# Kernel optimization log

Hardware: AMD Instinct MI355X
Metric: run time of the kernel (lower is better)

The kernel has to match this reference:

```python
import jax, jax.numpy as jnp
import numpy as np

D_MODEL = 256
INPUT_DIM = 63
NUM_CLASSES = 13
NUM_LAYERS = 4
D_STATE = 128
D_CONV = 4
D_INNER = 512          # expand * d_model
HEADDIM = 64
NHEADS = D_INNER // HEADDIM  # 8
NGROUPS = 1
CONV_DIM = D_INNER + 2 * NGROUPS * D_STATE   # 768
D_IN_PROJ = 2 * D_INNER + 2 * NGROUPS * D_STATE + NHEADS  # 1160
BATCH, SEQLEN = 8, 2048


def setup_inputs() -> dict:
    key = jax.random.key(0)
    ks = jax.random.split(key, 12)
    s = 0.02
    f32 = jnp.float32
    # dt_bias init as in mamba2: inverse-softplus of dt in [1e-3, 1e-1]
    dt = jnp.exp(jax.random.uniform(ks[6], (NUM_LAYERS, NHEADS), f32) * (np.log(0.1) - np.log(0.001)) + np.log(0.001))
    dt_bias = dt + jnp.log(-jnp.expm1(-dt))
    A_log = jnp.log(jax.random.uniform(ks[7], (NUM_LAYERS, NHEADS), f32, 1.0, 16.0))
    return {
        "x": jax.random.normal(ks[0], (BATCH, SEQLEN, INPUT_DIM), f32),
        "in_w": jax.random.normal(ks[1], (D_MODEL, INPUT_DIM), f32) * s,
        "in_b": jnp.zeros((D_MODEL,), f32),
        "ln_in_g": jnp.ones((D_MODEL,), f32),
        "ln_in_b": jnp.zeros((D_MODEL,), f32),
        "inproj_w": jax.random.normal(ks[2], (NUM_LAYERS, D_IN_PROJ, D_MODEL), f32) * s,
        "conv_w": jax.random.normal(ks[3], (NUM_LAYERS, CONV_DIM, D_CONV), f32) * 0.2,
        "conv_b": jnp.zeros((NUM_LAYERS, CONV_DIM), f32),
        "dt_bias": dt_bias,
        "A_log": A_log,
        "D": jnp.ones((NUM_LAYERS, NHEADS), f32),
        "norm_w": jnp.ones((NUM_LAYERS, D_INNER), f32),
        "outproj_w": jax.random.normal(ks[4], (NUM_LAYERS, D_MODEL, D_INNER), f32) * s,
        "ln_g": jnp.ones((NUM_LAYERS, D_MODEL), f32),
        "ln_b": jnp.zeros((NUM_LAYERS, D_MODEL), f32),
        "out_w": jax.random.normal(ks[5], (NUM_CLASSES, D_MODEL), f32) * s,
        "out_b": jnp.zeros((NUM_CLASSES,), f32),
    }


def layernorm(x, g, b, eps=1e-5):
    m = jnp.mean(x, -1, keepdims=True)
    v = jnp.mean(jnp.square(x - m), -1, keepdims=True)
    return (x - m) * jax.lax.rsqrt(v + eps) * g + b


def mamba2_block(x, w_in, cw, cb, dtb, Alog, Dp, nw, w_out):
    # x: (b, l, d_model)
    b, l, _ = x.shape
    zxbcdt = jnp.einsum('bld,ed->ble', x, w_in)                 # (b,l,1160)
    z = zxbcdt[..., :D_INNER]                                   # (b,l,512)
    xBC = zxbcdt[..., D_INNER:D_INNER + CONV_DIM]               # (b,l,768)
    dt = jax.nn.softplus(zxbcdt[..., D_INNER + CONV_DIM:] + dtb)  # (b,l,8)
    # causal depthwise conv1d + silu
    xp = jnp.pad(xBC, ((0, 0), (D_CONV - 1, 0), (0, 0)))
    kern = cw.T[:, None, :]                                     # (K,1,C)
    xBC = jax.lax.conv_general_dilated(
        xp, kern, (1,), 'VALID',
        dimension_numbers=('NWC', 'WIO', 'NWC'),
        feature_group_count=CONV_DIM)
    xBC = jax.nn.silu(xBC + cb)
    xin = xBC[..., :D_INNER].reshape(b, l, NHEADS, HEADDIM)     # (b,l,h,p)
    Bm = xBC[..., D_INNER:D_INNER + D_STATE]                    # (b,l,n)
    Cm = xBC[..., D_INNER + D_STATE:]                           # (b,l,n)
    A = -jnp.exp(Alog)                                          # (h,)
    dA = jnp.exp(dt * A)                                        # (b,l,h)
    dtx = dt[..., None] * xin                                   # (b,l,h,p)

    def step(state, inp):
        dA_t, dtx_t, B_t, C_t = inp                             # (b,h),(b,h,p),(b,n),(b,n)
        state = state * dA_t[..., None, None] + dtx_t[..., None] * B_t[:, None, None, :]
        y_t = jnp.einsum('bhpn,bn->bhp', state, C_t)
        return state, y_t

    state0 = jnp.zeros((b, NHEADS, HEADDIM, D_STATE), x.dtype)
    _, ys = jax.lax.scan(step, state0, (
        dA.transpose(1, 0, 2), dtx.transpose(1, 0, 2, 3),
        Bm.transpose(1, 0, 2), Cm.transpose(1, 0, 2)))
    y = ys.transpose(1, 0, 2, 3) + Dp[:, None] * xin            # (b,l,h,p)
    y = y.reshape(b, l, D_INNER)
    # gated RMSNorm (norm_before_gate=False): rmsnorm(y * silu(z)) * w
    y = y * jax.nn.silu(z)
    y = y * jax.lax.rsqrt(jnp.mean(jnp.square(y), -1, keepdims=True) + 1e-5) * nw
    return jnp.einsum('ble,de->bld', y, w_out)


def reference(x, in_w, in_b, ln_in_g, ln_in_b, inproj_w, conv_w, conv_b,
              dt_bias, A_log, D, norm_w, outproj_w, ln_g, ln_b, out_w, out_b):
    # input projection (dropout is identity in eval mode)
    h = layernorm(jnp.einsum('bli,di->bld', x, in_w) + in_b, ln_in_g, ln_in_b)
    for i in range(NUM_LAYERS):
        res = h
        h = mamba2_block(h, inproj_w[i], conv_w[i], conv_b[i], dt_bias[i],
                         A_log[i], D[i], norm_w[i], outproj_w[i])
        h = layernorm(h + res, ln_g[i], ln_b[i])
    logits = jnp.einsum('bld,cd->blc', h, out_w) + out_b
    return logits.transpose(1, 0, 2)  # (T, N, C) for CTC
```

## Files before the change

kernel.cpp:

```cpp
#include <hip/hip_runtime.h>
#include <math.h>


#define NTOK   16384
#define DMODEL 256
#define DINNER 512
#define DSTATE 128
#define NHEADS 8
#define HEADDIM 64
#define CONVDIM 768
#define DINPROJ 1288
#define NPADIN 1408
#define Q      128
#define NCHUNK 16
#define NBC    128

typedef __attribute__((ext_vector_type(8))) short bf16x8v;
typedef __attribute__((ext_vector_type(4))) float f32x4;
typedef __attribute__((ext_vector_type(8))) unsigned short ush8;
typedef __attribute__((ext_vector_type(4))) unsigned short ush4;

__device__ __forceinline__ float siluf_(float x){ return x / (1.f + expf(-x)); }

__device__ __forceinline__ unsigned short f2bf(float x){
  union { float f; unsigned u; } v; v.f = x;
  unsigned r = v.u + 0x7FFF + ((v.u >> 16) & 1);
  return (unsigned short)(r >> 16);
}
__device__ __forceinline__ float bf2f(unsigned short u){
  union { unsigned u; float f; } v; v.u = ((unsigned)u) << 16; return v.f;
}
__device__ __forceinline__ void g2lds16(const void* g, void* l){
  __builtin_amdgcn_global_load_lds(
      (const __attribute__((address_space(1))) unsigned int*)g,
      (__attribute__((address_space(3))) unsigned int*)l, 16, 0, 0);
}

__global__ __launch_bounds__(256) void k_cast_x(const float* __restrict__ x,
    unsigned short* __restrict__ xb){
  int idx = blockIdx.x*256 + threadIdx.x;
  int col = idx & 63, row = idx >> 6;
  xb[idx] = (col < 63) ? f2bf(x[(size_t)row*63 + col]) : 0;
}
__global__ __launch_bounds__(256) void k_cast_inw(const float* __restrict__ w,
    unsigned short* __restrict__ wb){
  int idx = blockIdx.x*256 + threadIdx.x;
  int k = idx & 63, n = idx >> 6;
  wb[idx] = (k < 63) ? f2bf(w[(size_t)n*63 + k]) : 0;
}
__global__ __launch_bounds__(256) void k_cast_pad(const float* __restrict__ w,
    unsigned short* __restrict__ wb, int Nsrc, int Npad, int K, int total){
  int idx = blockIdx.x*256 + threadIdx.x;
  if (idx >= total) return;
  int k = idx % K;
  int n = (idx / K) % Npad;
  int l = idx / (K*Npad);
  float v = (n < Nsrc) ? w[((size_t)l*Nsrc + n)*K + k] : 0.f;
  wb[idx] = f2bf(v);
}

__global__ __launch_bounds__(256) void gemm_ln(const unsigned short* __restrict__ A,
    const unsigned short* __restrict__ W, float* __restrict__ h,
    unsigned short* __restrict__ hb, const float* __restrict__ g,
    const float* __restrict__ be, int K, int addres){
  __shared__ unsigned short As[64*64];
  __shared__ unsigned short Ws[256*64];
  __shared__ float redS[4][64], redS2[4][64];
  int m0 = blockIdx.x * 64;
  int t = threadIdx.x;
  int wave = t >> 6, lane = t & 63;
  int lr = lane & 15, lk = lane >> 4;
  f32x4 acc[4][4] = {};
  for (int k0=0; k0<K; k0+=64){
    #pragma unroll
    for (int i=0;i<2;i++){
      int seg = i*256 + t;
      int row = seg >> 3, c8 = (seg&7)*8;
      g2lds16(A + (size_t)(m0+row)*K + k0 + c8, (char*)As + seg*16);
    }
    #pragma unroll
    for (int i=0;i<8;i++){
      int seg = i*256 + t;
      int row = seg >> 3, c8 = (seg&7)*8;
      g2lds16(W + (size_t)row*K + k0 + c8, (char*)Ws + seg*16);
    }
    __syncthreads();
    #pragma unroll
    for (int kk=0;kk<2;kk++){
      bf16x8v wf[4], af[4];
      #pragma unroll
      for (int ci=0;ci<4;ci++)
// ... 22 lines not shown
      }
      #pragma unroll
      for (int j=0;j<4;j++){ float v = acc[ci][ti][j]; pS[ti]+=v; pS2[ti]+=v*v; }
    }
  }
  #pragma unroll
  for (int ti=0;ti<4;ti++){
    pS[ti]  += __shfl_xor(pS[ti],16);  pS[ti]  += __shfl_xor(pS[ti],32);
    pS2[ti] += __shfl_xor(pS2[ti],16); pS2[ti] += __shfl_xor(pS2[ti],32);
  }
  if (lk == 0){
    #pragma unroll
    for (int ti=0;ti<4;ti++){ redS[wave][ti*16+lr] = pS[ti]; redS2[wave][ti*16+lr] = pS2[ti]; }
  }
  __syncthreads();
  #pragma unroll
  for (int ti=0;ti<4;ti++){
    int rloc = ti*16 + lr;
    float S  = redS[0][rloc]+redS[1][rloc]+redS[2][rloc]+redS[3][rloc];
    float S2 = redS2[0][rloc]+redS2[1][rloc]+redS2[2][rloc]+redS2[3][rloc];
    float mean = S*(1.f/256.f);
    float var  = S2*(1.f/256.f) - mean*mean;
    float r = rsqrtf(var + 1e-5f);
    int token = m0 + rloc;
    #pragma unroll
    for (int ci=0;ci<4;ci++){
      int col = wave*64 + ci*16 + lk*4;
      float o[4];
      #pragma unroll
      for (int j=0;j<4;j++) o[j] = (acc[ci][ti][j]-mean)*r*g[col+j] + be[col+j];
      *(float4*)&h[(size_t)token*256 + col] = make_float4(o[0],o[1],o[2],o[3]);
      ush4 ub = {f2bf(o[0]),f2bf(o[1]),f2bf(o[2]),f2bf(o[3])};
      *(ush4*)&hb[(size_t)token*256 + col] = ub;
    }
  }
}

__global__ __launch_bounds__(256) void gemm_in(const unsigned short* __restrict__ A,
    const unsigned short* __restrict__ W, unsigned short* __restrict__ zxb,
    const float* __restrict__ dt_bias, const float* __restrict__ A_log,
    float* __restrict__ dtg, float* __restrict__ Lag, float* __restrict__ Tg,
    float* __restrict__ wgb){
  __shared__ unsigned short As[128*64];
  __shared__ unsigned short Ws[128*64];
  int m0 = blockIdx.x * 128;
  int n0 = blockIdx.y * 128;
  int t = threadIdx.x;
  int wave = t >> 6, lane = t & 63;
  int wt = wave >> 1, wn = wave & 1;
  int lr = lane & 15, lk = lane >> 4;
  f32x4 acc[4][4] = {};
  for (int k0=0; k0<DMODEL; k0+=64){
    #pragma unroll
    for (int i=0;i<4;i++){
      int seg = i*256 + t;
      int row = seg >> 3, c8 = (seg&7)*8;
      g2lds16(A + (size_t)(m0+row)*DMODEL + k0 + c8, (char*)As + seg*16);
      g2lds16(W + (size_t)(n0+row)*DMODEL + k0 + c8, (char*)Ws + seg*16);
    }
    __syncthreads();
    #pragma unroll
    for (int kk=0;kk<2;kk++){
      bf16x8v wf[4], af[4];
      #pragma unroll
      for (int ci=0;ci<4;ci++)
        wf[ci] = *(const bf16x8v*)&Ws[(wn*64 + ci*16 + lr)*64 + kk*32 + lk*8];
      #pragma unroll
      for (int ti=0;ti<4;ti++)
        af[ti] = *(const bf16x8v*)&As[(wt*64 + ti*16 + lr)*64 + kk*32 + lk*8];
      #pragma unroll
      for (int ci=0;ci<4;ci++)
        #pragma unroll
        for (int ti=0;ti<4;ti++)
          acc[ci][ti] = __builtin_amdgcn_mfma_f32_16x16x32_bf16(wf[ci], af[ti], acc[ci][ti],0,0,0);
    }
    __syncthreads();
  }
  #pragma unroll
  for (int ci=0;ci<4;ci++){
    int col4 = n0 + wn*64 + ci*16 + lk*4;
    if (col4 < DINPROJ){
      #pragma unroll
      for (int ti=0;ti<4;ti++){
        int token = m0 + wt*64 + ti*16 + lr;
        ush4 ub = {f2bf(acc[ci][ti][0]),f2bf(acc[ci][ti][1]),
                   f2bf(acc[ci][ti][2]),f2bf(acc[ci][ti][3])};
        *(ush4*)&zxb[(size_t)token*DINPROJ + col4] = ub;
      }
    }
  }
  if (blockIdx.y == 10){
    float* dls = (float*)As;
    if (wn == 0 && lk < 2){
      #pragma unroll
      for (int ti=0;ti<4;ti++){
        int token = wt*64 + ti*16 + lr;
        #pragma unroll
        for (int j=0;j<4;j++) dls[token*8 + lk*4 + j] = acc[0][ti][j];
      }
    }
    __syncthreads();
    int bc = blockIdx.x;
    int rowc = m0;
    #pragma unroll
    for (int hi=0; hi<2; hi++){
      int hh = wave*2 + hi;
      float Aa = -expf(A_log[hh]);
      float bias = dt_bias[hh];
      int t0 = 2*lane, t1 = 2*lane+1;
      float r0v = dls[t0*8+hh] + bias;
      float r1v = dls[t1*8+hh] + bias;
      float d0 = (r0v > 20.f) ? r0v : log1pf(expf(r0v));
      float d1 = (r1v > 20.f) ? r1v : log1pf(expf(r1v));
      float v0 = d0*Aa, v1 = d1*Aa;
      float run = v0 + v1;
      #pragma unroll
      for (int off=1; off<64; off<<=1){
        float nb = __shfl_up(run, off);
        if (lane >= off) run += nb;
      }
      float La1 = run;
      float La0 = run - v1;
      float La_last = __shfl(run, 63);
      dtg[(size_t)(rowc+t0)*8 + hh] = d0;
      dtg[(size_t)(rowc+t1)*8 + hh] = d1;
      Lag[(size_t)(rowc+t0)*8 + hh] = La0;
      Lag[(size_t)(rowc+t1)*8 + hh] = La1;
      wgb[(size_t)(bc*8+hh)*Q + t0] = expf(La_last - La0) * d0;
      wgb[(size_t)(bc*8+hh)*Q + t1] = expf(La_last - La1) * d1;
      if (lane == 63) Tg[bc*8 + hh] = expf(La1);
    }
  }
}

__global__ __launch_bounds__(256) void k_conv(const unsigned short* __restrict__ zxb,
    const float* __restrict__ cw, const float* __restrict__ cb,
    unsigned short* __restrict__ xbcb, unsigned short* __restrict__ Xt,
    unsigned short* __restrict__ Bt){
  int tid = threadIdx.x;
  int c0 = (blockIdx.x * 8 + (tid & 7)) * 8;
  int tg = blockIdx.y * 32 + (tid >> 3);
  int r0 = tg * 8;
  int l0 = r0 & 2047;
  float kw[4][8], bias[8];
  #pragma unroll
  for (int j=0;j<8;j++){
    float4 k4 = *(const float4*)&cw[(c0+j)*4];
    kw[0][j]=k4.x; kw[1][j]=k4.y; kw[2][j]=k4.z; kw[3][j]=k4.w;
    bias[j] = cb[c0+j];
  }
  float zv[11][8];
  #pragma unroll
  for (int i=0;i<11;i++){
    if (l0 - 3 + i >= 0){
      ush8 v = *(const ush8*)&zxb[(size_t)(r0-3+i)*DINPROJ + 512 + c0];
      #pragma unroll
      for (int j=0;j<8;j++) zv[i][j] = bf2f(v[j]);
    } else {
      #pragma unroll
      for (int j=0;j<8;j++) zv[i][j] = 0.f;
    }
  }
  unsigned short ob[8][8];
  #pragma unroll
  for (int tt=0;tt<8;tt++){
    #pragma unroll
    for (int j=0;j<8;j++){
      float acc = bias[j] + zv[tt][j]*kw[0][j] + zv[tt+1][j]*kw[1][j]
                + zv[tt+2][j]*kw[2][j] + zv[tt+3][j]*kw[3][j];
      ob[tt][j] = f2bf(siluf_(acc));
    }
    *(ush8*)&xbcb[(size_t)(r0+tt)*CONVDIM + c0] = *(ush8*)ob[tt];
  }
  if (c0 < 640){
    int bc = r0 >> 7, s0 = r0 & 127;
    #pragma unroll
    for (int j=0;j<8;j++){
      ush8 col = {ob[0][j],ob[1][j],ob[2][j],ob[3][j],ob[4][j],ob[5][j],ob[6][j],ob[7][j]};
      int d = c0 + j;
      unsigned short* dst = (d < 512)
          ? (Xt + ((size_t)bc*512 + d)*Q + s0)
          : (Bt + ((size_t)bc*128 + (d-512))*Q + s0);
      *(ush8*)dst = col;
    }
  }
}

__global__ __launch_bounds__(256) void k_cbp1(const unsigned short* __restrict__ xbcb,
    const unsigned short* __restrict__ Bt, const unsigned short* __restrict__ Xt,
    const float* __restrict__ wg, unsigned short* __restrict__ CBb,
    float* __restrict__ states){
  __shared__ char smem[52736];
  int tid = threadIdx.x;
  int bc = blockIdx.x;
  int wave = tid >> 6, lane = tid & 63;
  int lr = lane & 15, lk = lane >> 4;
  if (blockIdx.y == 8){
    unsigned short* Cs = (unsigned short*)smem;
    unsigned short* Bs = (unsigned short*)(smem + 16384);
    int rowc = bc * Q;
    int wS = wave >> 1, wT = wave & 1;
    f32x4 acc[4][4] = {};
    for (int k0 = 0; k0 < DSTATE; k0 += 64){
      #pragma unroll
      for (int i=0;i<4;i++){
        int seg = i*256 + tid;
        int row = seg >> 3;
        int c8  = (seg & 7) * 8;
        g2lds16(xbcb + (size_t)(rowc+row)*CONVDIM + 640 + k0 + c8, Cs + seg*8);
        g2lds16(xbcb + (size_t)(rowc+row)*CONVDIM + 512 + k0 + c8, Bs + seg*8);
      }
      __syncthreads();
      #pragma unroll
      for (int kk=0; kk<2; kk++){
        bf16x8v bS[4], cT[4];
        #pragma unroll
        for (int si=0;si<4;si++)
          bS[si] = *(const bf16x8v*)&Bs[(wS*64 + si*16 + lr)*64 + kk*32 + lk*8];
        #pragma unroll
        for (int ti=0;ti<4;ti++)
          cT[ti] = *(const bf16x8v*)&Cs[(wT*64 + ti*16 + lr)*64 + kk*32 + lk*8];
        #pragma unroll
        for (int si=0;si<4;si++)
          #pragma unroll
// ... 28 lines not shown
      int n = seg >> 4;
      int s8 = (seg & 15) * 8;
      ush8 u = *(const ush8*)&Bt[(size_t)bc*128*Q + n*Q + s8];
      ush8 o;
      #pragma unroll
      for (int j=0;j<8;j++) o[j] = f2bf(bf2f(u[j]) * wv[s8+j]);
      *(ush8*)&Bw[n*136 + s8] = o;
    }
    #pragma unroll
    for (int it=0; it<4; it++){
      int seg = it*256 + tid;
      int p = seg >> 4;
      int s8 = (seg & 15) * 8;
      *(ush8*)&Xs[p*136 + s8] = *(const ush8*)&Xt[(size_t)bc*512*Q + (h*64+p)*Q + s8];
    }
    __syncthreads();
    int wn = wave >> 1, wp = wave & 1;
    f32x4 acc[4][2] = {};
    #pragma unroll
    for (int ks=0; ks<4; ks++){
      bf16x8v a[4], x[2];
      #pragma unroll
      for (int mi=0;mi<4;mi++)
        a[mi] = *(const bf16x8v*)&Bw[(wn*64 + mi*16 + lr)*136 + ks*32 + lk*8];
      #pragma unroll
      for (int ni=0;ni<2;ni++)
        x[ni] = *(const bf16x8v*)&Xs[(wp*32 + ni*16 + lr)*136 + ks*32 + lk*8];
      #pragma unroll
      for (int mi=0;mi<4;mi++)
        #pragma unroll
        for (int ni=0;ni<2;ni++)
          acc[mi][ni] = __builtin_amdgcn_mfma_f32_16x16x32_bf16(a[mi], x[ni], acc[mi][ni], 0, 0, 0);
    }
    float* st = states + ((size_t)(b*8+h)*16 + c) * (DSTATE*HEADDIM);
    #pragma unroll
    for (int mi=0;mi<4;mi++)
      #pragma unroll
      for (int ni=0;ni<2;ni++){
        int p = wp*32 + ni*16 + lr;
        int nb = wn*64 + mi*16 + lk*4;
        *(f32x4*)&st[p*DSTATE + nb] = acc[mi][ni];
      }
  }
}

__global__ __launch_bounds__(256) void k_pass2(const float* __restrict__ states,
    const float* __restrict__ T, unsigned short* __restrict__ st0b){
  int e = blockIdx.x*256 + threadIdx.x;
  int bh = e >> 13;
  int np = e & 8191;
  int b = bh >> 3, h = bh & 7;
  size_t base = (size_t)bh * NCHUNK * 8192 + np;
  float run = 0.f;
  #pragma unroll
  for (int c=0; c<NCHUNK; c++){
    float g = states[base + (size_t)c*8192];
    st0b[base + (size_t)c*8192] = f2bf(run);
    run = fmaf(T[(b*NCHUNK+c)*8 + h], run, g);
  }
}

__global__ __launch_bounds__(256) void k_pass3(const unsigned short* __restrict__ xbcb,
    const unsigned short* __restrict__ Xt, const unsigned short* __restrict__ CBb,
    const unsigned short* __restrict__ st0b, const float* __restrict__ dt,
    const float* __restrict__ La, unsigned short* __restrict__ yssmb){
  int bc = blockIdx.x, h = blockIdx.y;
  int b = bc >> 4, c = bc & 15;
  int rowc = bc * Q;
  int tid = threadIdx.x;
  __shared__ unsigned short bufA[128*136];
  __shared__ unsigned short bufB[64*136];
  __shared__ float La_s[Q], dt_s[Q], eLa_s[Q];
  if (tid < Q){
    float Lv = La[(size_t)(rowc+tid)*8 + h];
    La_s[tid] = Lv;
    dt_s[tid] = dt[(size_t)(rowc+tid)*8 + h];
    eLa_s[tid] = expf(Lv);
  }
  #pragma unroll
  for (int it=0; it<8; it++){
    int seg = it*256 + tid;
    int tt = seg >> 4;
    int n8 = (seg & 15) * 8;
    *(ush8*)&bufA[tt*136 + n8] = *(const ush8*)&xbcb[(size_t)(rowc+tt)*CONVDIM + 640 + n8];
  }
  const unsigned short* S0 = st0b + ((size_t)(b*8+h)*16 + c) * 8192;
  #pragma unroll
  for (int it=0; it<4; it++){
    int seg = it*256 + tid;
// ... 50 lines not shown
  for (int it=0; it<4; it++){
    int seg = it*256 + tid;
    int p = seg >> 4;
    int s8 = (seg & 15) * 8;
    *(ush8*)&bufB[p*136 + s8] = *(const ush8*)&Xt[(size_t)bc*512*Q + (h*64+p)*Q + s8];
  }
  __syncthreads();
  #pragma unroll
  for (int ks=0; ks<4; ks++){
    bf16x8v xf[2], mf[4];
    #pragma unroll
    for (int pi=0;pi<2;pi++)
      xf[pi] = *(const bf16x8v*)&bufB[(wp*32 + pi*16 + lr)*136 + ks*32 + lk*8];
    #pragma unroll
    for (int ti=0;ti<4;ti++)
      mf[ti] = *(const bf16x8v*)&bufA[(wt*64 + ti*16 + lr)*136 + ks*32 + lk*8];
    #pragma unroll
    for (int pi=0;pi<2;pi++)
      #pragma unroll
      for (int ti=0;ti<4;ti++)
        acc[pi][ti] = __builtin_amdgcn_mfma_f32_16x16x32_bf16(xf[pi], mf[ti], acc[pi][ti],0,0,0);
  }
  #pragma unroll
  for (int pi=0;pi<2;pi++){
    int p4 = wp*32 + pi*16 + lk*4;
    #pragma unroll
    for (int ti=0;ti<4;ti++){
      int tt = wt*64 + ti*16 + lr;
      ush4 ub = {f2bf(acc[pi][ti][0]),f2bf(acc[pi][ti][1]),
                 f2bf(acc[pi][ti][2]),f2bf(acc[pi][ti][3])};
      *(ush4*)&yssmb[(size_t)(rowc+tt)*DINNER + h*64 + p4] = ub;
    }
  }
}

__global__ __launch_bounds__(64) void k_gate_norm(const unsigned short* __restrict__ yssmb,
    const unsigned short* __restrict__ xbcb, const unsigned short* __restrict__ zxb,
    const float* __restrict__ Dp, const float* __restrict__ nw,
    unsigned short* __restrict__ outb){
  int row = blockIdx.x;
  int t = threadIdx.x;
  int d0 = t*8;
  ush8 ys = *(const ush8*)&yssmb[(size_t)row*DINNER + d0];
  ush8 xi = *(const ush8*)&xbcb[(size_t)row*CONVDIM + d0];
  ush8 z8 = *(const ush8*)&zxb[(size_t)row*DINPROJ + d0];
  float Dh = Dp[d0 >> 6];
  float v[8];
  float s2 = 0.f;
  #pragma unroll
  for (int j=0;j<8;j++){
    v[j] = fmaf(Dh, bf2f(xi[j]), bf2f(ys[j])) * siluf_(bf2f(z8[j]));
    s2 += v[j]*v[j];
  }
  #pragma unroll
  for (int off=1; off<64; off<<=1) s2 += __shfl_xor(s2, off);
  float r = rsqrtf(s2*(1.f/512.f) + 1e-5f);
  unsigned short ub[8];
  #pragma unroll
  for (int j=0;j<8;j++) ub[j] = f2bf(v[j]*r*nw[d0+j]);
  *(ush8*)&outb[(size_t)row*DINNER + d0] = *(ush8*)ub;
}

__global__ __launch_bounds__(256) void k_logits(const unsigned short* __restrict__ hb,
    const float* __restrict__ ow, const float* __restrict__ ob,
    float* __restrict__ out){
  int idx = blockIdx.x*256 + threadIdx.x;
  if (idx >= 2048*8*13) return;
  int c = idx % 13;
  int bb = (idx/13) & 7;
  int l = idx / 104;
  const ush8* hr = (const ush8*)(hb + (size_t)(bb*2048 + l)*256);
  const float4* wr = (const float4*)(ow + c*256);
  float acc = ob[c];
  #pragma unroll 4
  for (int d=0; d<32; d++){
    ush8 a = hr[d];
    float4 w0 = wr[d*2], w1 = wr[d*2+1];
    acc += bf2f(a[0])*w0.x + bf2f(a[1])*w0.y + bf2f(a[2])*w0.z + bf2f(a[3])*w0.w
         + bf2f(a[4])*w1.x + bf2f(a[5])*w1.y + bf2f(a[6])*w1.z + bf2f(a[7])*w1.w;
  }
  out[idx] = acc;
}

extern "C" void kernel_launch(void* const* d_in, const int* in_sizes, int n_in,
                              void* d_out, int out_size, void* d_ws, size_t ws_size,
                              hipStream_t stream) {
  const float* x        = (const float*)d_in[0];
  const float* in_w     = (const float*)d_in[1];
  const float* ln_in_g  = (const float*)d_in[3];
  const float* ln_in_b  = (const float*)d_in[4];
  const float* inproj_w = (const float*)d_in[5];
  const float* conv_w   = (const float*)d_in[6];
  const float* conv_b   = (const float*)d_in[7];
  const float* dt_bias  = (const float*)d_in[8];
  const float* A_log    = (const float*)d_in[9];
  const float* Dp       = (const float*)d_in[10];
  const float* norm_w   = (const float*)d_in[11];
  const float* outproj_w= (const float*)d_in[12];
  const float* ln_g     = (const float*)d_in[13];
  const float* ln_b     = (const float*)d_in[14];
  const float* out_w    = (const float*)d_in[15];
  const float* out_b    = (const float*)d_in[16];

  float* ws = (float*)d_ws;
  float* h      = ws;
  float* dtg    = ws + 4325376;
  float* Lag    = ws + 4456448;
  float* Tg     = ws + 4587520;
  float* wg     = ws + 4588544;
  float* statesF= ws + 5637120;
  unsigned short* zxb   = (unsigned short*)(ws + 14025728);
  unsigned short* xbcb  = (unsigned short*)(ws + 24577024);
  unsigned short* Xt    = (unsigned short*)(ws + 30868480);
  unsigned short* Bt    = (unsigned short*)(ws + 35062784);
  unsigned short* CBb   = (unsigned short*)(ws + 36111360);
  unsigned short* st0b  = (unsigned short*)(ws + 37159936);
  unsigned short* yssmb = (unsigned short*)(ws + 41354240);
  unsigned short* ynormb= (unsigned short*)(ws + 45548544);
  unsigned short* hb    = (unsigned short*)(ws + 49742848);
  unsigned short* xb    = (unsigned short*)(ws + 51840000);
  unsigned short* wxb   = (unsigned short*)(ws + 52364288);
  unsigned short* wbin  = (unsigned short*)(ws + 52372480);
  unsigned short* wbout = (unsigned short*)(ws + 53093376);

  k_cast_x<<<NTOK*64/256, 256, 0, stream>>>(x, xb);
  k_cast_inw<<<DMODEL*64/256, 256, 0, stream>>>(in_w, wxb);
  k_cast_pad<<<(4*NPADIN*DMODEL + 255)/256, 256, 0, stream>>>(
      inproj_w, wbin, DINPROJ, NPADIN, DMODEL, 4*NPADIN*DMODEL);
  k_cast_pad<<<(4*DMODEL*DINNER + 255)/256, 256, 0, stream>>>(
      outproj_w, wbout, DMODEL, DMODEL, DINNER, 4*DMODEL*DINNER);
  gemm_ln<<<NTOK/64, 256, 0, stream>>>(xb, wxb, h, hb, ln_in_g, ln_in_b, 64, 0);

  for (int i=0; i<4; i++){
    gemm_in<<<dim3(NTOK/128, NPADIN/128), 256, 0, stream>>>(
        hb, wbin + (size_t)i*NPADIN*DMODEL, zxb,
        dt_bias + i*NHEADS, A_log + i*NHEADS, dtg, Lag, Tg, wg);
    k_conv<<<dim3(12, 64), 256, 0, stream>>>(zxb, conv_w + (size_t)i*CONVDIM*4,
        conv_b + i*CONVDIM, xbcb, Xt, Bt);
    k_cbp1<<<dim3(NBC, 9), 256, 0, stream>>>(xbcb, Bt, Xt, wg, CBb, statesF);
    k_pass2<<<2048, 256, 0, stream>>>(statesF, Tg, st0b);
    k_pass3<<<dim3(NBC, NHEADS), 256, 0, stream>>>(xbcb, Xt, CBb, st0b, dtg, Lag, yssmb);
    k_gate_norm<<<NTOK, 64, 0, stream>>>(yssmb, xbcb, zxb, Dp + i*NHEADS,
        norm_w + i*DINNER, ynormb);
    gemm_ln<<<NTOK/64, 256, 0, stream>>>(ynormb, wbout + (size_t)i*DMODEL*DINNER,
        h, hb, ln_g + i*DMODEL, ln_b + i*DMODEL, 512, 1);
  }

  k_logits<<<(2048*8*13 + 255)/256, 256, 0, stream>>>(hb, out_w, out_b, (float*)d_out);
}
```

Before: 617.3 us.

## Fuse depthwise conv into in-projection GEMM epilogue and merge cast kernels

The causal depthwise conv plus SiLU is computed inside the in-projection GEMM epilogue for the xBC column tiles, reading the tile from shared memory. The three preceding rows come from a small recomputed dot product against the previous tokens' hidden state, so the full zxbcdt intermediate no longer needs to be written to and re-read from global memory. Only z is stored, in a compact buffer. This removes the separate k_conv launch and its traffic, and the four weight/input cast kernels are merged into one launch. The cost is extra shared memory, a scalar halo recompute, and a heavier epilogue in the GEMM.

```diff
diff --git a/kernel.cpp b/kernel.cpp
--- a/kernel.cpp
+++ b/kernel.cpp
@@ -36,27 +36,33 @@
       (__attribute__((address_space(3))) unsigned int*)l, 16, 0, 0);
 }
 
-__global__ __launch_bounds__(256) void k_cast_x(const float* __restrict__ x,
-    unsigned short* __restrict__ xb){
+__global__ __launch_bounds__(256) void k_cast_all(const float* __restrict__ x,
+    const float* __restrict__ in_w, const float* __restrict__ inproj_w,
+    const float* __restrict__ outproj_w, unsigned short* __restrict__ xb,
+    unsigned short* __restrict__ wxb, unsigned short* __restrict__ wbin,
+    unsigned short* __restrict__ wbout){
   int idx = blockIdx.x*256 + threadIdx.x;
-  int col = idx & 63, row = idx >> 6;
-  xb[idx] = (col < 63) ? f2bf(x[(size_t)row*63 + col]) : 0;
-}
-__global__ __launch_bounds__(256) void k_cast_inw(const float* __restrict__ w,
-    unsigned short* __restrict__ wb){
-  int idx = blockIdx.x*256 + threadIdx.x;
-  int k = idx & 63, n = idx >> 6;
-  wb[idx] = (k < 63) ? f2bf(w[(size_t)n*63 + k]) : 0;
-}
-__global__ __launch_bounds__(256) void k_cast_pad(const float* __restrict__ w,
-    unsigned short* __restrict__ wb, int Nsrc, int Npad, int K, int total){
-  int idx = blockIdx.x*256 + threadIdx.x;
-  if (idx >= total) return;
-  int k = idx % K;
-  int n = (idx / K) % Npad;
-  int l = idx / (K*Npad);
-  float v = (n < Nsrc) ? w[((size_t)l*Nsrc + n)*K + k] : 0.f;
-  wb[idx] = f2bf(v);
+  if (idx < 1048576){
+    int col = idx & 63, row = idx >> 6;
+    xb[idx] = (col < 63) ? f2bf(x[(size_t)row*63 + col]) : 0;
+    return;
+  }
+  idx -= 1048576;
+  if (idx < 16384){
+    int k = idx & 63, n = idx >> 6;
+    wxb[idx] = (k < 63) ? f2bf(in_w[(size_t)n*63 + k]) : 0;
+    return;
+  }
+  idx -= 16384;
+  if (idx < 1441792){
+    int k = idx & 255;
+    int n = (idx >> 8) % NPADIN;
+    int l = idx / (256*NPADIN);
+    wbin[idx] = (n < DINPROJ) ? f2bf(inproj_w[((size_t)l*DINPROJ + n)*256 + k]) : 0;
+    return;
+  }
+  idx -= 1441792;
+  if (idx < 524288) wbout[idx] = f2bf(outproj_w[idx]);
 }
 
 __global__ __launch_bounds__(256) void gemm_ln(const unsigned short* __restrict__ A,
@@ -150,12 +156,16 @@
 }
 
 __global__ __launch_bounds__(256) void gemm_in(const unsigned short* __restrict__ A,
-    const unsigned short* __restrict__ W, unsigned short* __restrict__ zxb,
+    const unsigned short* __restrict__ W, unsigned short* __restrict__ zb,
+    unsigned short* __restrict__ xbcb, unsigned short* __restrict__ Xt,
+    unsigned short* __restrict__ Bt,
+    const float* __restrict__ cw, const float* __restrict__ cb,
     const float* __restrict__ dt_bias, const float* __restrict__ A_log,
     float* __restrict__ dtg, float* __restrict__ Lag, float* __restrict__ Tg,
     float* __restrict__ wgb){
-  __shared__ unsigned short As[128*64];
-  __shared__ unsigned short Ws[128*64];
+  __shared__ char smem[37376];
+  unsigned short* As = (unsigned short*)smem;
+  unsigned short* Ws = (unsigned short*)(smem + 16384);
   int m0 = blockIdx.x * 128;
   int n0 = blockIdx.y * 128;
   int t = threadIdx.x;
@@ -189,21 +199,99 @@
     }
     __syncthreads();
   }
-  #pragma unroll
-  for (int ci=0;ci<4;ci++){
-    int col4 = n0 + wn*64 + ci*16 + lk*4;
-    if (col4 < DINPROJ){
+  int ytile = blockIdx.y;
+  if (ytile < 4){
+    #pragma unroll
+    for (int ci=0;ci<4;ci++){
+      int col4 = n0 + wn*64 + ci*16 + lk*4;
       #pragma unroll
       for (int ti=0;ti<4;ti++){
         int token = m0 + wt*64 + ti*16 + lr;
         ush4 ub = {f2bf(acc[ci][ti][0]),f2bf(acc[ci][ti][1]),
                    f2bf(acc[ci][ti][2]),f2bf(acc[ci][ti][3])};
-        *(ush4*)&zxb[(size_t)token*DINPROJ + col4] = ub;
-      }
-    }
-  }
-  if (blockIdx.y == 10){
-    float* dls = (float*)As;
+        *(ush4*)&zb[(size_t)token*512 + col4] = ub;
+      }
+    }
+  } else if (ytile < 10){
+    unsigned short* zraw = (unsigned short*)smem;
+    unsigned short* hb3  = (unsigned short*)(smem + 35632);
+    bool haveprev = (m0 & 2047) != 0;
+    if (t < 96){
+      int r = t >> 5, c8 = (t & 31) * 8;
+      ush8 v = {0,0,0,0,0,0,0,0};
+      if (haveprev) v = *(const ush8*)&A[(size_t)(m0-3+r)*DMODEL + c8];
+      *(ush8*)&hb3[r*256 + c8] = v;
+    }
+    #pragma unroll
+    for (int ci=0;ci<4;ci++){
+      int cl = wn*64 + ci*16 + lk*4;
+      #pragma unroll
+      for (int ti=0;ti<4;ti++){
+        int tl = wt*64 + ti*16 + lr;
+        ush4 ub = {f2bf(acc[ci][ti][0]),f2bf(acc[ci][ti][1]),
+                   f2bf(acc[ci][ti][2]),f2bf(acc[ci][ti][3])};
+        *(ush4*)&zraw[(tl+3)*136 + cl] = ub;
+      }
+    }
+    __syncthreads();
+    for (int idx = t; idx < 384; idx += 256){
+      int r = idx >> 7, c = idx & 127;
+      float dot = 0.f;
+      if (haveprev){
+        const ush8* wr8 = (const ush8*)&W[(size_t)(n0+c)*DMODEL];
+        const ush8* hr8 = (const ush8*)&hb3[r*256];
+        #pragma unroll 8
+        for (int k8=0;k8<32;k8++){
+          ush8 wv = wr8[k8], hv = hr8[k8];
+          #pragma unroll
+          for (int j=0;j<8;j++) dot += bf2f(hv[j]) * bf2f(wv[j]);
+        }
+      }
+      zraw[r*136 + c] = f2bf(dot);
+    }
+    __syncthreads();
+    int cl0 = (t & 15)*8;
+    int tl0 = (t >> 4)*8;
+    int ch0 = (n0 - 512) + cl0;
+    float kw[4][8], bias[8];
+    #pragma unroll
+    for (int j=0;j<8;j++){
+      float4 k4 = *(const float4*)&cw[(ch0+j)*4];
+      kw[0][j]=k4.x; kw[1][j]=k4.y; kw[2][j]=k4.z; kw[3][j]=k4.w;
+      bias[j] = cb[ch0+j];
+    }
+    float zv[11][8];
+    #pragma unroll
+    for (int i=0;i<11;i++){
+      ush8 v = *(const ush8*)&zraw[(tl0+i)*136 + cl0];
+      #pragma unroll
+      for (int j=0;j<8;j++) zv[i][j] = bf2f(v[j]);
+    }
+    unsigned short ob[8][8];
+    #pragma unroll
+    for (int tt=0;tt<8;tt++){
+      #pragma unroll
+      for (int j=0;j<8;j++){
+        float a = bias[j] + zv[tt][j]*kw[0][j] + zv[tt+1][j]*kw[1][j]
+                + zv[tt+2][j]*kw[2][j] + zv[tt+3][j]*kw[3][j];
+        ob[tt][j] = f2bf(siluf_(a));
+      }
+      *(ush8*)&xbcb[(size_t)(m0+tl0+tt)*CONVDIM + ch0] = *(ush8*)ob[tt];
+    }
+    if (ch0 < 640){
+      int bc = m0 >> 7;
+      #pragma unroll
+      for (int j=0;j<8;j++){
+        int d = ch0 + j;
+        ush8 col = {ob[0][j],ob[1][j],ob[2][j],ob[3][j],ob[4][j],ob[5][j],ob[6][j],ob[7][j]};
+        unsigned short* dst = (d < 512)
+            ? (Xt + ((size_t)bc*512 + d)*Q + tl0)
+            : (Bt + ((size_t)bc*128 + (d-512))*Q + tl0);
+        *(ush8*)dst = col;
+      }
+    }
+  } else {
+    float* dls = (float*)smem;
     if (wn == 0 && lk < 2){
       #pragma unroll
       for (int ti=0;ti<4;ti++){
@@ -242,59 +330,6 @@
       wgb[(size_t)(bc*8+hh)*Q + t0] = expf(La_last - La0) * d0;
       wgb[(size_t)(bc*8+hh)*Q + t1] = expf(La_last - La1) * d1;
       if (lane == 63) Tg[bc*8 + hh] = expf(La1);
-    }
-  }
-}
-
-__global__ __launch_bounds__(256) void k_conv(const unsigned short* __restrict__ zxb,
-    const float* __restrict__ cw, const float* __restrict__ cb,
-    unsigned short* __restrict__ xbcb, unsigned short* __restrict__ Xt,
-    unsigned short* __restrict__ Bt){
-  int tid = threadIdx.x;
-  int c0 = (blockIdx.x * 8 + (tid & 7)) * 8;
-  int tg = blockIdx.y * 32 + (tid >> 3);
-  int r0 = tg * 8;
-  int l0 = r0 & 2047;
-  float kw[4][8], bias[8];
-  #pragma unroll
-  for (int j=0;j<8;j++){
-    float4 k4 = *(const float4*)&cw[(c0+j)*4];
-    kw[0][j]=k4.x; kw[1][j]=k4.y; kw[2][j]=k4.z; kw[3][j]=k4.w;
-    bias[j] = cb[c0+j];
-  }
-  float zv[11][8];
-  #pragma unroll
-  for (int i=0;i<11;i++){
-    if (l0 - 3 + i >= 0){
-      ush8 v = *(const ush8*)&zxb[(size_t)(r0-3+i)*DINPROJ + 512 + c0];
-      #pragma unroll
-      for (int j=0;j<8;j++) zv[i][j] = bf2f(v[j]);
-    } else {
-      #pragma unroll
-      for (int j=0;j<8;j++) zv[i][j] = 0.f;
-    }
-  }
-  unsigned short ob[8][8];
-  #pragma unroll
-  for (int tt=0;tt<8;tt++){
-    #pragma unroll
-    for (int j=0;j<8;j++){
-      float acc = bias[j] + zv[tt][j]*kw[0][j] + zv[tt+1][j]*kw[1][j]
-                + zv[tt+2][j]*kw[2][j] + zv[tt+3][j]*kw[3][j];
-      ob[tt][j] = f2bf(siluf_(acc));
-    }
-    *(ush8*)&xbcb[(size_t)(r0+tt)*CONVDIM + c0] = *(ush8*)ob[tt];
-  }
-  if (c0 < 640){
-    int bc = r0 >> 7, s0 = r0 & 127;
-    #pragma unroll
-    for (int j=0;j<8;j++){
-      ush8 col = {ob[0][j],ob[1][j],ob[2][j],ob[3][j],ob[4][j],ob[5][j],ob[6][j],ob[7][j]};
-      int d = c0 + j;
-      unsigned short* dst = (d < 512)
-          ? (Xt + ((size_t)bc*512 + d)*Q + s0)
-          : (Bt + ((size_t)bc*128 + (d-512))*Q + s0);
-      *(ush8*)dst = col;
     }
   }
 }
@@ -539,7 +574,7 @@
 }
 
 __global__ __launch_bounds__(64) void k_gate_norm(const unsigned short* __restrict__ yssmb,
-    const unsigned short* __restrict__ xbcb, const unsigned short* __restrict__ zxb,
+    const unsigned short* __restrict__ xbcb, const unsigned short* __restrict__ zb,
     const float* __restrict__ Dp, const float* __restrict__ nw,
     unsigned short* __restrict__ outb){
   int row = blockIdx.x;
@@ -547,7 +582,7 @@
   int d0 = t*8;
   ush8 ys = *(const ush8*)&yssmb[(size_t)row*DINNER + d0];
   ush8 xi = *(const ush8*)&xbcb[(size_t)row*CONVDIM + d0];
-  ush8 z8 = *(const ush8*)&zxb[(size_t)row*DINPROJ + d0];
+  ush8 z8 = *(const ush8*)&zb[(size_t)row*512 + d0];
   float Dh = Dp[d0 >> 6];
   float v[8];
   float s2 = 0.f;
@@ -608,43 +643,38 @@
 
   float* ws = (float*)d_ws;
   float* h      = ws;
-  float* dtg    = ws + 4325376;
-  float* Lag    = ws + 4456448;
-  float* Tg     = ws + 4587520;
-  float* wg     = ws + 4588544;
-  float* statesF= ws + 5637120;
-  unsigned short* zxb   = (unsigned short*)(ws + 14025728);
-  unsigned short* xbcb  = (unsigned short*)(ws + 24577024);
-  unsigned short* Xt    = (unsigned short*)(ws + 30868480);
-  unsigned short* Bt    = (unsigned short*)(ws + 35062784);
-  unsigned short* CBb   = (unsigned short*)(ws + 36111360);
-  unsigned short* st0b  = (unsigned short*)(ws + 37159936);
-  unsigned short* yssmb = (unsigned short*)(ws + 41354240);
-  unsigned short* ynormb= (unsigned short*)(ws + 45548544);
-  unsigned short* hb    = (unsigned short*)(ws + 49742848);
-  unsigned short* xb    = (unsigned short*)(ws + 51840000);
-  unsigned short* wxb   = (unsigned short*)(ws + 52364288);
-  unsigned short* wbin  = (unsigned short*)(ws + 52372480);
-  unsigned short* wbout = (unsigned short*)(ws + 53093376);
-
-  k_cast_x<<<NTOK*64/256, 256, 0, stream>>>(x, xb);
-  k_cast_inw<<<DMODEL*64/256, 256, 0, stream>>>(in_w, wxb);
-  k_cast_pad<<<(4*NPADIN*DMODEL + 255)/256, 256, 0, stream>>>(
-      inproj_w, wbin, DINPROJ, NPADIN, DMODEL, 4*NPADIN*DMODEL);
-  k_cast_pad<<<(4*DMODEL*DINNER + 255)/256, 256, 0, stream>>>(
-      outproj_w, wbout, DMODEL, DMODEL, DINNER, 4*DMODEL*DINNER);
+  float* dtg    = ws +  4194304;
+  float* Lag    = ws +  4325376;
+  float* Tg     = ws +  4456448;
+  float* wg     = ws +  4457472;
+  float* statesF= ws +  5506048;
+  unsigned short* zb    = (unsigned short*)(ws + 13894656);
+  unsigned short* xbcb  = (unsigned short*)(ws + 18088960);
+  unsigned short* Xt    = (unsigned short*)(ws + 24380416);
+  unsigned short* Bt    = (unsigned short*)(ws + 28574720);
+  unsigned short* CBb   = (unsigned short*)(ws + 29623296);
+  unsigned short* st0b  = (unsigned short*)(ws + 30671872);
+  unsigned short* yssmb = (unsigned short*)(ws + 34866176);
+  unsigned short* ynormb= (unsigned short*)(ws + 39060480);
+  unsigned short* hb    = (unsigned short*)(ws + 43254784);
+  unsigned short* xb    = (unsigned short*)(ws + 45351936);
+  unsigned short* wxb   = (unsigned short*)(ws + 45876224);
+  unsigned short* wbin  = (unsigned short*)(ws + 45884416);
+  unsigned short* wbout = (unsigned short*)(ws + 46605312);
+
+  k_cast_all<<<11840, 256, 0, stream>>>(x, in_w, inproj_w, outproj_w,
+      xb, wxb, wbin, wbout);
   gemm_ln<<<NTOK/64, 256, 0, stream>>>(xb, wxb, h, hb, ln_in_g, ln_in_b, 64, 0);
 
   for (int i=0; i<4; i++){
-    gemm_in<<<dim3(NTOK/128, NPADIN/128), 256, 0, stream>>>(
-        hb, wbin + (size_t)i*NPADIN*DMODEL, zxb,
+    gemm_in<<<dim3(NTOK/128, 11), 256, 0, stream>>>(
+        hb, wbin + (size_t)i*NPADIN*DMODEL, zb, xbcb, Xt, Bt,
+        conv_w + (size_t)i*CONVDIM*4, conv_b + i*CONVDIM,
         dt_bias + i*NHEADS, A_log + i*NHEADS, dtg, Lag, Tg, wg);
-    k_conv<<<dim3(12, 64), 256, 0, stream>>>(zxb, conv_w + (size_t)i*CONVDIM*4,
-        conv_b + i*CONVDIM, xbcb, Xt, Bt);
     k_cbp1<<<dim3(NBC, 9), 256, 0, stream>>>(xbcb, Bt, Xt, wg, CBb, statesF);
     k_pass2<<<2048, 256, 0, stream>>>(statesF, Tg, st0b);
     k_pass3<<<dim3(NBC, NHEADS), 256, 0, stream>>>(xbcb, Xt, CBb, st0b, dtg, Lag, yssmb);
-    k_gate_norm<<<NTOK, 64, 0, stream>>>(yssmb, xbcb, zxb, Dp + i*NHEADS,
+    k_gate_norm<<<NTOK, 64, 0, stream>>>(yssmb, xbcb, zb, Dp + i*NHEADS,
         norm_w + i*DINNER, ynormb);
     gemm_ln<<<NTOK/64, 256, 0, stream>>>(ynormb, wbout + (size_t)i*DMODEL*DINNER,
         h, hb, ln_g + i*DMODEL, ln_b + i*DMODEL, 512, 1);
```

Result: slower. 703.3 us (+13.9%).

## Fuse gated RMSNorm into out-proj GEMM, bf16 chunk states, merge cast kernels

Applied to the files above, without the earlier changes.

Folds the gated RMSNorm (D-skip, SiLU gate, RMS scaling) into the out-projection GEMM prologue. The normalized activations for a 64-token tile are built straight in LDS, which removes the ynormb round trip and one launch per layer. Per-chunk SSM states are stored as bf16 instead of fp32, halving that traffic at some cost in precision. The four weight and input cast kernels become one launch, and the in-proj grid drops from 11 to 11 column tiles explicitly (NPADIN/128 = 11), so the grid is unchanged. The fused GEMM uses a large LDS footprint (64 KB A plus 32 KB W), which may limit occupancy.

```diff
diff --git a/kernel.cpp b/kernel.cpp
--- a/kernel.cpp
+++ b/kernel.cpp
@@ -36,27 +36,33 @@
       (__attribute__((address_space(3))) unsigned int*)l, 16, 0, 0);
 }
 
-__global__ __launch_bounds__(256) void k_cast_x(const float* __restrict__ x,
-    unsigned short* __restrict__ xb){
+__global__ __launch_bounds__(256) void k_cast_all(const float* __restrict__ x,
+    const float* __restrict__ in_w, const float* __restrict__ inproj_w,
+    const float* __restrict__ outproj_w, unsigned short* __restrict__ xb,
+    unsigned short* __restrict__ wxb, unsigned short* __restrict__ wbin,
+    unsigned short* __restrict__ wbout){
   int idx = blockIdx.x*256 + threadIdx.x;
-  int col = idx & 63, row = idx >> 6;
-  xb[idx] = (col < 63) ? f2bf(x[(size_t)row*63 + col]) : 0;
-}
-__global__ __launch_bounds__(256) void k_cast_inw(const float* __restrict__ w,
-    unsigned short* __restrict__ wb){
-  int idx = blockIdx.x*256 + threadIdx.x;
-  int k = idx & 63, n = idx >> 6;
-  wb[idx] = (k < 63) ? f2bf(w[(size_t)n*63 + k]) : 0;
-}
-__global__ __launch_bounds__(256) void k_cast_pad(const float* __restrict__ w,
-    unsigned short* __restrict__ wb, int Nsrc, int Npad, int K, int total){
-  int idx = blockIdx.x*256 + threadIdx.x;
-  if (idx >= total) return;
-  int k = idx % K;
-  int n = (idx / K) % Npad;
-  int l = idx / (K*Npad);
-  float v = (n < Nsrc) ? w[((size_t)l*Nsrc + n)*K + k] : 0.f;
-  wb[idx] = f2bf(v);
+  if (idx < 1048576){
+    int col = idx & 63, row = idx >> 6;
+    xb[idx] = (col < 63) ? f2bf(x[(size_t)row*63 + col]) : 0;
+    return;
+  }
+  idx -= 1048576;
+  if (idx < 16384){
+    int k = idx & 63, n = idx >> 6;
+    wxb[idx] = (k < 63) ? f2bf(in_w[(size_t)n*63 + k]) : 0;
+    return;
+  }
+  idx -= 16384;
+  if (idx < 1441792){
+    int k = idx & 255;
+    int n = (idx >> 8) % NPADIN;
+    int l = idx / (256*NPADIN);
+    wbin[idx] = (n < DINPROJ) ? f2bf(inproj_w[((size_t)l*DINPROJ + n)*256 + k]) : 0;
+    return;
+  }
+  idx -= 1441792;
+  if (idx < 524288) wbout[idx] = f2bf(outproj_w[idx]);
 }
 
 __global__ __launch_bounds__(256) void gemm_ln(const unsigned short* __restrict__ A,
@@ -145,6 +151,128 @@
       *(float4*)&h[(size_t)token*256 + col] = make_float4(o[0],o[1],o[2],o[3]);
       ush4 ub = {f2bf(o[0]),f2bf(o[1]),f2bf(o[2]),f2bf(o[3])};
       *(ush4*)&hb[(size_t)token*256 + col] = ub;
+    }
+  }
+}
+
+__global__ __launch_bounds__(256) void gemm_gln(
+    const unsigned short* __restrict__ yssmb, const unsigned short* __restrict__ xbcb,
+    const unsigned short* __restrict__ zxb, const float* __restrict__ Dp,
+    const float* __restrict__ nw, const unsigned short* __restrict__ W,
+    float* __restrict__ h, unsigned short* __restrict__ hb,
+    const float* __restrict__ g, const float* __restrict__ be){
+  __shared__ unsigned short As[8*64*64];
+  __shared__ unsigned short Ws[256*64];
+  __shared__ float redS[4][64], redS2[4][64];
+  int m0 = blockIdx.x * 64;
+  int t = threadIdx.x;
+  int row = t >> 2, seg = t & 3;
+  int token = m0 + row;
+  int k0s = seg * 128;
+  float Dh0 = Dp[seg*2], Dh1 = Dp[seg*2 + 1];
+  float s2 = 0.f;
+  #pragma unroll
+  for (int i=0;i<16;i++){
+    int k = k0s + i*8;
+    ush8 ys = *(const ush8*)&yssmb[(size_t)token*DINNER + k];
+    ush8 xi = *(const ush8*)&xbcb[(size_t)token*CONVDIM + k];
+    ush8 z8 = *(const ush8*)&zxb[(size_t)token*DINPROJ + k];
+    float Dhh = (i < 8) ? Dh0 : Dh1;
+    unsigned short vb[8];
+    #pragma unroll
+    for (int j=0;j<8;j++){
+      float v = fmaf(Dhh, bf2f(xi[j]), bf2f(ys[j])) * siluf_(bf2f(z8[j]));
+      s2 += v*v;
+      vb[j] = f2bf(v);
+    }
+    *(ush8*)&As[(k>>6)*4096 + row*64 + (k&63)] = *(ush8*)vb;
+  }
+  s2 += __shfl_xor(s2, 1);
+  s2 += __shfl_xor(s2, 2);
+  float rn = rsqrtf(s2*(1.f/512.f) + 1e-5f);
+  #pragma unroll
+  for (int i=0;i<16;i++){
+    int k = k0s + i*8;
+    unsigned short* ap = &As[(k>>6)*4096 + row*64 + (k&63)];
+    ush8 vv = *(ush8*)ap;
+    float4 w0 = *(const float4*)&nw[k];
+    float4 w1 = *(const float4*)&nw[k+4];
+    float nwv[8] = {w0.x,w0.y,w0.z,w0.w,w1.x,w1.y,w1.z,w1.w};
+    unsigned short vb[8];
+    #pragma unroll
+    for (int j=0;j<8;j++) vb[j] = f2bf(bf2f(vv[j]) * rn * nwv[j]);
+    *(ush8*)ap = *(ush8*)vb;
+  }
+  __syncthreads();
+  int wave = t >> 6, lane = t & 63;
+  int lr = lane & 15, lk = lane >> 4;
+  f32x4 acc[4][4] = {};
+  for (int k0=0; k0<512; k0+=64){
+    #pragma unroll
+    for (int i=0;i<8;i++){
+      int sg = i*256 + t;
+      int rw = sg >> 3, c8 = (sg&7)*8;
+      g2lds16(W + (size_t)rw*DINNER + k0 + c8, (char*)Ws + sg*16);
+    }
+    __syncthreads();
+    #pragma unroll
+    for (int kk=0;kk<2;kk++){
+      bf16x8v wf[4], af[4];
+      #pragma unroll
+      for (int ci=0;ci<4;ci++)
+        wf[ci] = *(const bf16x8v*)&Ws[(wave*64 + ci*16 + lr)*64 + kk*32 + lk*8];
+      #pragma unroll
+      for (int ti=0;ti<4;ti++)
+        af[ti] = *(const bf16x8v*)&As[(k0>>6)*4096 + (ti*16 + lr)*64 + kk*32 + lk*8];
+      #pragma unroll
+      for (int ci=0;ci<4;ci++)
+        #pragma unroll
+        for (int ti=0;ti<4;ti++)
+          acc[ci][ti] = __builtin_amdgcn_mfma_f32_16x16x32_bf16(wf[ci], af[ti], acc[ci][ti],0,0,0);
+    }
+    __syncthreads();
+  }
+  float pS[4] = {}, pS2[4] = {};
+  #pragma unroll
+  for (int ci=0;ci<4;ci++){
+    int col = wave*64 + ci*16 + lk*4;
+    #pragma unroll
+    for (int ti=0;ti<4;ti++){
+      int tok = m0 + ti*16 + lr;
+      float4 r4 = *(const float4*)&h[(size_t)tok*256 + col];
+      acc[ci][ti][0]+=r4.x; acc[ci][ti][1]+=r4.y; acc[ci][ti][2]+=r4.z; acc[ci][ti][3]+=r4.w;
+      #pragma unroll
+      for (int j=0;j<4;j++){ float v = acc[ci][ti][j]; pS[ti]+=v; pS2[ti]+=v*v; }
+    }
+  }
+  #pragma unroll
+  for (int ti=0;ti<4;ti++){
+    pS[ti]  += __shfl_xor(pS[ti],16);  pS[ti]  += __shfl_xor(pS[ti],32);
+    pS2[ti] += __shfl_xor(pS2[ti],16); pS2[ti] += __shfl_xor(pS2[ti],32);
+  }
+  if (lk == 0){
+    #pragma unroll
+    for (int ti=0;ti<4;ti++){ redS[wave][ti*16+lr] = pS[ti]; redS2[wave][ti*16+lr] = pS2[ti]; }
+  }
+  __syncthreads();
+  #pragma unroll
+  for (int ti=0;ti<4;ti++){
+    int rloc = ti*16 + lr;
+    float S  = redS[0][rloc]+redS[1][rloc]+redS[2][rloc]+redS[3][rloc];
+    float S2 = redS2[0][rloc]+redS2[1][rloc]+redS2[2][rloc]+redS2[3][rloc];
+    float mean = S*(1.f/256.f);
+    float var  = S2*(1.f/256.f) - mean*mean;
+    float r = rsqrtf(var + 1e-5f);
+    int tok = m0 + rloc;
+    #pragma unroll
+    for (int ci=0;ci<4;ci++){
+      int col = wave*64 + ci*16 + lk*4;
+      float o[4];
+      #pragma unroll
+      for (int j=0;j<4;j++) o[j] = (acc[ci][ti][j]-mean)*r*g[col+j] + be[col+j];
+      *(float4*)&h[(size_t)tok*256 + col] = make_float4(o[0],o[1],o[2],o[3]);
+      ush4 ub = {f2bf(o[0]),f2bf(o[1]),f2bf(o[2]),f2bf(o[3])};
+      *(ush4*)&hb[(size_t)tok*256 + col] = ub;
     }
   }
 }
@@ -302,7 +430,7 @@
 __global__ __launch_bounds__(256) void k_cbp1(const unsigned short* __restrict__ xbcb,
     const unsigned short* __restrict__ Bt, const unsigned short* __restrict__ Xt,
     const float* __restrict__ wg, unsigned short* __restrict__ CBb,
-    float* __restrict__ states){
+    unsigned short* __restrict__ statesB){
   __shared__ char smem[52736];
   int tid = threadIdx.x;
   int bc = blockIdx.x;
@@ -397,19 +525,21 @@
         for (int ni=0;ni<2;ni++)
           acc[mi][ni] = __builtin_amdgcn_mfma_f32_16x16x32_bf16(a[mi], x[ni], acc[mi][ni], 0, 0, 0);
     }
-    float* st = states + ((size_t)(b*8+h)*16 + c) * (DSTATE*HEADDIM);
+    unsigned short* st = statesB + ((size_t)(b*8+h)*16 + c) * (DSTATE*HEADDIM);
     #pragma unroll
     for (int mi=0;mi<4;mi++)
       #pragma unroll
       for (int ni=0;ni<2;ni++){
         int p = wp*32 + ni*16 + lr;
         int nb = wn*64 + mi*16 + lk*4;
-        *(f32x4*)&st[p*DSTATE + nb] = acc[mi][ni];
+        ush4 ub = {f2bf(acc[mi][ni][0]),f2bf(acc[mi][ni][1]),
+                   f2bf(acc[mi][ni][2]),f2bf(acc[mi][ni][3])};
+        *(ush4*)&st[p*DSTATE + nb] = ub;
       }
   }
 }
 
-__global__ __launch_bounds__(256) void k_pass2(const float* __restrict__ states,
+__global__ __launch_bounds__(256) void k_pass2(const unsigned short* __restrict__ statesB,
     const float* __restrict__ T, unsigned short* __restrict__ st0b){
   int e = blockIdx.x*256 + threadIdx.x;
   int bh = e >> 13;
@@ -419,7 +549,7 @@
   float run = 0.f;
   #pragma unroll
   for (int c=0; c<NCHUNK; c++){
-    float g = states[base + (size_t)c*8192];
+    float g = bf2f(statesB[base + (size_t)c*8192]);
     st0b[base + (size_t)c*8192] = f2bf(run);
     run = fmaf(T[(b*NCHUNK+c)*8 + h], run, g);
   }
@@ -536,33 +666,6 @@
       *(ush4*)&yssmb[(size_t)(rowc+tt)*DINNER + h*64 + p4] = ub;
     }
   }
-}
-
-__global__ __launch_bounds__(64) void k_gate_norm(const unsigned short* __restrict__ yssmb,
-    const unsigned short* __restrict__ xbcb, const unsigned short* __restrict__ zxb,
-    const float* __restrict__ Dp, const float* __restrict__ nw,
-    unsigned short* __restrict__ outb){
-  int row = blockIdx.x;
-  int t = threadIdx.x;
-  int d0 = t*8;
-  ush8 ys = *(const ush8*)&yssmb[(size_t)row*DINNER + d0];
-  ush8 xi = *(const ush8*)&xbcb[(size_t)row*CONVDIM + d0];
-  ush8 z8 = *(const ush8*)&zxb[(size_t)row*DINPROJ + d0];
-  float Dh = Dp[d0 >> 6];
-  float v[8];
-  float s2 = 0.f;
-  #pragma unroll
-  for (int j=0;j<8;j++){
-    v[j] = fmaf(Dh, bf2f(xi[j]), bf2f(ys[j])) * siluf_(bf2f(z8[j]));
-    s2 += v[j]*v[j];
-  }
-  #pragma unroll
-  for (int off=1; off<64; off<<=1) s2 += __shfl_xor(s2, off);
-  float r = rsqrtf(s2*(1.f/512.f) + 1e-5f);
-  unsigned short ub[8];
-  #pragma unroll
-  for (int j=0;j<8;j++) ub[j] = f2bf(v[j]*r*nw[d0+j]);
-  *(ush8*)&outb[(size_t)row*DINNER + d0] = *(ush8*)ub;
 }
 
 __global__ __launch_bounds__(256) void k_logits(const unsigned short* __restrict__ hb,
@@ -608,46 +711,40 @@
 
   float* ws = (float*)d_ws;
   float* h      = ws;
-  float* dtg    = ws + 4325376;
-  float* Lag    = ws + 4456448;
-  float* Tg     = ws + 4587520;
-  float* wg     = ws + 4588544;
-  float* statesF= ws + 5637120;
-  unsigned short* zxb   = (unsigned short*)(ws + 14025728);
-  unsigned short* xbcb  = (unsigned short*)(ws + 24577024);
-  unsigned short* Xt    = (unsigned short*)(ws + 30868480);
-  unsigned short* Bt    = (unsigned short*)(ws + 35062784);
-  unsigned short* CBb   = (unsigned short*)(ws + 36111360);
-  unsigned short* st0b  = (unsigned short*)(ws + 37159936);
-  unsigned short* yssmb = (unsigned short*)(ws + 41354240);
-  unsigned short* ynormb= (unsigned short*)(ws + 45548544);
-  unsigned short* hb    = (unsigned short*)(ws + 49742848);
-  unsigned short* xb    = (unsigned short*)(ws + 51840000);
-  unsigned short* wxb   = (unsigned short*)(ws + 52364288);
-  unsigned short* wbin  = (unsigned short*)(ws + 52372480);
-  unsigned short* wbout = (unsigned short*)(ws + 53093376);
-
-  k_cast_x<<<NTOK*64/256, 256, 0, stream>>>(x, xb);
-  k_cast_inw<<<DMODEL*64/256, 256, 0, stream>>>(in_w, wxb);
-  k_cast_pad<<<(4*NPADIN*DMODEL + 255)/256, 256, 0, stream>>>(
-      inproj_w, wbin, DINPROJ, NPADIN, DMODEL, 4*NPADIN*DMODEL);
-  k_cast_pad<<<(4*DMODEL*DINNER + 255)/256, 256, 0, stream>>>(
-      outproj_w, wbout, DMODEL, DMODEL, DINNER, 4*DMODEL*DINNER);
+  float* dtg    = ws +  4194304;
+  float* Lag    = ws +  4325376;
+  float* Tg     = ws +  4456448;
+  float* wg     = ws +  4457472;
+  unsigned short* statesB = (unsigned short*)(ws +  5506048);
+  unsigned short* st0b    = (unsigned short*)(ws +  9700352);
+  unsigned short* zxb     = (unsigned short*)(ws + 13894656);
+  unsigned short* xbcb    = (unsigned short*)(ws + 24445952);
+  unsigned short* Xt      = (unsigned short*)(ws + 30737408);
+  unsigned short* Bt      = (unsigned short*)(ws + 34931712);
+  unsigned short* CBb     = (unsigned short*)(ws + 35980288);
+  unsigned short* yssmb   = (unsigned short*)(ws + 37028864);
+  unsigned short* hb      = (unsigned short*)(ws + 41223168);
+  unsigned short* xb      = (unsigned short*)(ws + 43320320);
+  unsigned short* wxb     = (unsigned short*)(ws + 43844608);
+  unsigned short* wbin    = (unsigned short*)(ws + 43852800);
+  unsigned short* wbout   = (unsigned short*)(ws + 44573696);
+
+  k_cast_all<<<11840, 256, 0, stream>>>(x, in_w, inproj_w, outproj_w,
+      xb, wxb, wbin, wbout);
   gemm_ln<<<NTOK/64, 256, 0, stream>>>(xb, wxb, h, hb, ln_in_g, ln_in_b, 64, 0);
 
   for (int i=0; i<4; i++){
-    gemm_in<<<dim3(NTOK/128, NPADIN/128), 256, 0, stream>>>(
+    gemm_in<<<dim3(NTOK/128, 11), 256, 0, stream>>>(
         hb, wbin + (size_t)i*NPADIN*DMODEL, zxb,
         dt_bias + i*NHEADS, A_log + i*NHEADS, dtg, Lag, Tg, wg);
     k_conv<<<dim3(12, 64), 256, 0, stream>>>(zxb, conv_w + (size_t)i*CONVDIM*4,
         conv_b + i*CONVDIM, xbcb, Xt, Bt);
-    k_cbp1<<<dim3(NBC, 9), 256, 0, stream>>>(xbcb, Bt, Xt, wg, CBb, statesF);
-    k_pass2<<<2048, 256, 0, stream>>>(statesF, Tg, st0b);
+    k_cbp1<<<dim3(NBC, 9), 256, 0, stream>>>(xbcb, Bt, Xt, wg, CBb, statesB);
+    k_pass2<<<2048, 256, 0, stream>>>(statesB, Tg, st0b);
     k_pass3<<<dim3(NBC, NHEADS), 256, 0, stream>>>(xbcb, Xt, CBb, st0b, dtg, Lag, yssmb);
-    k_gate_norm<<<NTOK, 64, 0, stream>>>(yssmb, xbcb, zxb, Dp + i*NHEADS,
-        norm_w + i*DINNER, ynormb);
-    gemm_ln<<<NTOK/64, 256, 0, stream>>>(ynormb, wbout + (size_t)i*DMODEL*DINNER,
-        h, hb, ln_g + i*DMODEL, ln_b + i*DMODEL, 512, 1);
+    gemm_gln<<<NTOK/64, 256, 0, stream>>>(yssmb, xbcb, zxb, Dp + i*NHEADS,
+        norm_w + i*DINNER, wbout + (size_t)i*DMODEL*DINNER,
+        h, hb, ln_g + i*DMODEL, ln_b + i*DMODEL);
   }
 
   k_logits<<<(2048*8*13 + 255)/256, 256, 0, stream>>>(hb, out_w, out_b, (float*)d_out);
```

After: 628.7 us. Within noise of the previous version (+1.8%).
